# Kernel optimization log

Hardware: AMD Instinct MI355X
Metric: run time of the kernel (lower is better)

## Reference

```python
import jax, jax.numpy as jnp
import numpy as np

N_NODES = 100000


def _sage_conv(x, src, dst, W_l, W_r, b, num_nodes):
    # PyG SAGEConv with mean aggregation:
    # out_i = (mean_{j: (j->i) in E} x_j) @ W_l + x_i @ W_r + b
    msg_sum = jax.ops.segment_sum(x[src], dst, num_segments=num_nodes)  # [N, F]
    deg = jax.ops.segment_sum(jnp.ones_like(src, dtype=x.dtype), dst, num_segments=num_nodes)
    agg = msg_sum / jnp.maximum(deg, 1.0)[:, None]
    return agg @ W_l + x @ W_r + b


def setup_inputs() -> dict:
    key = jax.random.key(0)
    k = jax.random.split(key, 7)
    F_IN, H, C = 128, 128, 14
    E = 1600000
    x = jax.random.normal(k[0], (N_NODES, F_IN), dtype=jnp.float32)
    edge_index = jax.random.randint(k[1], (2, E), 0, N_NODES, dtype=jnp.int64)
    s = 1.0 / np.sqrt(F_IN)
    W1_l = jax.random.normal(k[2], (F_IN, H), dtype=jnp.float32) * s
    W1_r = jax.random.normal(k[3], (F_IN, H), dtype=jnp.float32) * s
    b1 = jnp.zeros((H,), dtype=jnp.float32)
    sh = 1.0 / np.sqrt(H)
    W2_l = jax.random.normal(k[4], (H, C), dtype=jnp.float32) * sh
    W2_r = jax.random.normal(k[5], (H, C), dtype=jnp.float32) * sh
    b2 = jnp.zeros((C,), dtype=jnp.float32)
    return {"x": x, "edge_index": edge_index, "edge_SF_num": 6,
            "W1_l": W1_l, "W1_r": W1_r, "b1": b1,
            "W2_l": W2_l, "W2_r": W2_r, "b2": b2}


def reference(x, edge_index, edge_SF_num, W1_l, W1_r, b1, W2_l, W2_r, b2):
    src, dst = edge_index[0], edge_index[1]
    h = _sage_conv(x, src, dst, W1_l, W1_r, b1, N_NODES)
    h = jax.nn.relu(h)
    # dropout is identity at inference (training=False)
    out = _sage_conv(h, src, dst, W2_l, W2_r, b2, N_NODES)
    x_SF = jax.nn.log_softmax(out[:, :edge_SF_num], axis=1)
    x_Ptx = jax.nn.log_softmax(out[:, edge_SF_num:], axis=1)
    return (x_SF, x_Ptx)
```

## Files before the change

### kernel.cpp

```cpp
#include <hip/hip_runtime.h>
#include <hip/hip_bf16.h>

#define NN 100000
#define F 128
#define C_OUT 14
#define ZP 16
#define WIN 64
#define NWIN ((NN + WIN - 1) / WIN)
#define WCAP 1408
#define EBATCH 4096
#define HS 136

typedef __attribute__((ext_vector_type(8))) short v8s;
typedef __attribute__((ext_vector_type(4))) float v4f;
typedef __attribute__((ext_vector_type(2))) float v2f;

static __device__ __forceinline__ unsigned short f2bf(float f) {
    unsigned int u = __float_as_uint(f);
    unsigned int r = (u + 0x7fffu + ((u >> 16) & 1u)) >> 16;
    return (unsigned short)r;
}
static __device__ __forceinline__ unsigned int pack2(float a, float b) {
    return (unsigned int)f2bf(a) | ((unsigned int)f2bf(b) << 16);
}
static __device__ __forceinline__ void unpack2(unsigned int u, float& lo, float& hi) {
    lo = __uint_as_float(u << 16);
    hi = __uint_as_float(u & 0xffff0000u);
}
static __device__ __forceinline__ void accf8(const uint2 u, float* a) {
    v2f f0 = __builtin_amdgcn_cvt_pk_f32_fp8((int)u.x, false);
    a[0] += f0[0]; a[1] += f0[1];
    v2f f1 = __builtin_amdgcn_cvt_pk_f32_fp8((int)u.x, true);
    a[2] += f1[0]; a[3] += f1[1];
    v2f f2 = __builtin_amdgcn_cvt_pk_f32_fp8((int)u.y, false);
    a[4] += f2[0]; a[5] += f2[1];
    v2f f3 = __builtin_amdgcn_cvt_pk_f32_fp8((int)u.y, true);
    a[6] += f3[0]; a[7] += f3[1];
}
static __device__ __forceinline__ unsigned int bf4_to_fp8x4(const unsigned short* sp) {
    float f0, f1, f2, f3;
    unpack2(*(const unsigned int*)(sp + 0), f0, f1);
    unpack2(*(const unsigned int*)(sp + 2), f2, f3);
    unsigned int w = __builtin_amdgcn_cvt_pk_fp8_f32(f0, f1, 0, false);
    return __builtin_amdgcn_cvt_pk_fp8_f32(f2, f3, w, true);
}

__global__ __launch_bounds__(256) void bin_kernel(
    const int* __restrict__ src, const int* __restrict__ dst,
    unsigned* __restrict__ bucket, int* __restrict__ wcur, int E)
{
    __shared__ int cnt_s[NWIN];
    __shared__ int gbase_s[NWIN];
    const int t = threadIdx.x;
    for (int w = t; w < NWIN; w += 256) cnt_s[w] = 0;
    __syncthreads();

    int      wreg[16];
    unsigned ereg[16];
    const int e0 = blockIdx.x * EBATCH;
    #pragma unroll
    for (int j = 0; j < 16; ++j) {
        const int e = e0 + j * 256 + t;
        int w = -1; unsigned ent = 0;
        if (e < E) {
            const int d = dst[e];
            const int s = src[e];
            w   = d >> 6;
            ent = ((unsigned)(d & (WIN - 1)) << 17) | (unsigned)s;
            atomicAdd(&cnt_s[w], 1);
        }
        wreg[j] = w; ereg[j] = ent;
    }
    __syncthreads();
    for (int w = t; w < NWIN; w += 256) {
        const int c = cnt_s[w];
        gbase_s[w] = c ? atomicAdd(&wcur[w], c) : 0;
    }
    __syncthreads();
    for (int w = t; w < NWIN; w += 256) cnt_s[w] = 0;
    __syncthreads();
    #pragma unroll
    for (int j = 0; j < 16; ++j) {
        const int w = wreg[j];
        if (w >= 0) {
            const int pos = gbase_s[w] + atomicAdd(&cnt_s[w], 1);
            if (pos < WCAP) bucket[(size_t)w * WCAP + pos] = ereg[j];
        }
    }
}

__global__ __launch_bounds__(256) void wprep_kernel(
    const float* __restrict__ W1l, const float* __restrict__ W1r,
    const float* __restrict__ W2l, const float* __restrict__ W2r,
    unsigned short* __restrict__ Wb, unsigned short* __restrict__ W2t)
{
    const int idx = blockIdx.x * 256 + threadIdx.x;
    if (idx < 2 * 128 * 128) {
        const int c   = idx >> 14;
        const int rem = idx & 16383;
        const int n   = rem >> 7;
        const int k   = rem & 127;
        const float* W = c ? W1r : W1l;
        Wb[idx] = f2bf(W[k * 128 + n]);
    } else if (idx < 2 * 128 * 128 + 32 * 128) {
        const int j = idx - 2 * 128 * 128;
        const int n = j >> 7;
        const int k = j & 127;
        float wv = 0.0f;
        if (n < 16) { if (n < C_OUT) wv = W2l[k * C_OUT + n]; }
        else        { if (n - 16 < C_OUT) wv = W2r[k * C_OUT + (n - 16)]; }
        W2t[j] = f2bf(wv);
    }
}

#define KS 72
__global__ __launch_bounds__(256, 2) void pre1_kernel(
    const float* __restrict__ x, const unsigned short* __restrict__ Wb,
    const float* __restrict__ b1, unsigned char* __restrict__ pqa,
    unsigned short* __restrict__ pqs)
{
    __shared__ unsigned short lds[128 * KS + 256 * KS];
    unsigned short* A_s = lds;
    unsigned short* W_s = lds + 128 * KS;

    const int t    = threadIdx.x;
    const int m0   = blockIdx.x * 128;
    const int lane = t & 63;
    const int wave = t >> 6;
    const int lr   = lane & 15;
    const int quad = lane >> 4;
    const int nw0  = wave * 64;

    v4f acc[8][4];
    #pragma unroll
    for (int mt = 0; mt < 8; ++mt)
        #pragma unroll
        for (int nt = 0; nt < 4; ++nt)
            acc[mt][nt] = (v4f){0.f, 0.f, 0.f, 0.f};

    #pragma unroll
    for (int ph = 0; ph < 2; ++ph) {
        const int kh = ph * 64;
        if (ph) __syncthreads();

        {
            const int mi = t & 127;
            const int ko = (t >> 7) * 32;
            const int m  = m0 + mi;
            unsigned short* dp = &A_s[mi * KS + ko];
            if (m < NN) {
                const float4* sp = (const float4*)(x + (size_t)m * F + kh + ko);
                #pragma unroll
                for (int j = 0; j < 8; j += 2) {
                    const float4 f0 = sp[j], f1 = sp[j + 1];
                    uint4 o;
                    o.x = pack2(f0.x, f0.y); o.y = pack2(f0.z, f0.w);
                    o.z = pack2(f1.x, f1.y); o.w = pack2(f1.z, f1.w);
                    *(uint4*)(dp + j * 4) = o;
                }
            } else {
                #pragma unroll
                for (int j = 0; j < 4; ++j)
                    *(uint4*)(dp + j * 8) = make_uint4(0u, 0u, 0u, 0u);
            }
        }
        {
            const unsigned short* sp = Wb + (size_t)t * 128 + kh;
            unsigned short* dp = &W_s[t * KS];
            #pragma unroll
            for (int j = 0; j < 8; ++j)
                *(uint4*)(dp + j * 8) = *(const uint4*)(sp + j * 8);
        }
        __syncthreads();

        #pragma unroll
        for (int ks = 0; ks < 2; ++ks) {
            const int k0 = ks * 32 + quad * 8;
            const v8s b0 = *(const v8s*)&W_s[(nw0 +  0 + lr) * KS + k0];
            const v8s b1v= *(const v8s*)&W_s[(nw0 + 16 + lr) * KS + k0];
            const v8s b2 = *(const v8s*)&W_s[(nw0 + 32 + lr) * KS + k0];
            const v8s b3 = *(const v8s*)&W_s[(nw0 + 48 + lr) * KS + k0];
            #pragma unroll
            for (int mt = 0; mt < 8; ++mt) {
                const v8s a = *(const v8s*)&A_s[(mt * 16 + lr) * KS + k0];
                acc[mt][0] = __builtin_amdgcn_mfma_f32_16x16x32_bf16(a, b0,  acc[mt][0], 0, 0, 0);
                acc[mt][1] = __builtin_amdgcn_mfma_f32_16x16x32_bf16(a, b1v, acc[mt][1], 0, 0, 0);
                acc[mt][2] = __builtin_amdgcn_mfma_f32_16x16x32_bf16(a, b2,  acc[mt][2], 0, 0, 0);
                acc[mt][3] = __builtin_amdgcn_mfma_f32_16x16x32_bf16(a, b3,  acc[mt][3], 0, 0, 0);
            }
        }
        __syncthreads();
    }

    float bias[4];
    #pragma unroll
    for (int nt = 0; nt < 4; ++nt) {
        const int n = nw0 + nt * 16 + lr;
        bias[nt] = (n >= 128) ? b1[n - 128] : 0.0f;
    }

    unsigned short* C_s = lds;
    #pragma unroll
    for (int p = 0; p < 2; ++p) {
        if ((nw0 >> 7) == p) {
            #pragma unroll
            for (int mt = 0; mt < 8; ++mt)
                #pragma unroll
                for (int nt = 0; nt < 4; ++nt) {
                    const int n = (nw0 & 127) + nt * 16 + lr;
                    #pragma unroll
                    for (int r = 0; r < 4; ++r) {
                        const int m = mt * 16 + quad * 4 + r;
                        C_s[m * 136 + n] = f2bf(acc[mt][nt][r] + bias[nt]);
                    }
                }
        }
        __syncthreads();
        if (p == 0) {
            const int mi8 = t >> 1;
            const int c0  = (t & 1) * 64;
            const int m   = m0 + mi8;
            if (m < NN) {
                unsigned char* dp = pqa + (size_t)m * 128 + c0;
                #pragma unroll
                for (int j = 0; j < 4; ++j) {
                    const unsigned short* sp = &C_s[mi8 * 136 + c0 + j * 16];
                    uint4 w;
                    w.x = bf4_to_fp8x4(sp + 0);
                    w.y = bf4_to_fp8x4(sp + 4);
                    w.z = bf4_to_fp8x4(sp + 8);
                    w.w = bf4_to_fp8x4(sp + 12);
                    *(uint4*)(dp + j * 16) = w;
                }
            }
        } else {
            const int mi = t & 127;
            const int nh = (t >> 7) * 64;
            const int m  = m0 + mi;
            if (m < NN) {
                unsigned short* dp = pqs + (size_t)m * 128 + nh;
                const unsigned short* sp = &C_s[mi * 136 + nh];
                #pragma unroll
                for (int j = 0; j < 8; ++j)
                    *(uint4*)(dp + j * 8) = *(const uint4*)(sp + j * 8);
            }
        }
        __syncthreads();
    }
}

__global__ __launch_bounds__(256, 5) void agg1f_kernel(
    const unsigned char* __restrict__ pqa, const unsigned short* __restrict__ pqs,
    unsigned* __restrict__ bucket, const int* __restrict__ wcur,
    const unsigned short* __restrict__ W2t, const float* __restrict__ b2,
    int* __restrict__ wbase, unsigned short* __restrict__ z, float* __restrict__ r)
{
    __shared__ unsigned list[WCAP];
    __shared__ int cnt_s[WIN], base_s[WIN], cur_s[WIN];
    __shared__ unsigned short hsm[WIN * HS];
    __shared__ unsigned short W2s[32 * HS];
    const int t  = threadIdx.x;
    const int wb = blockIdx.x;
    const int cntw = min(wcur[wb], WCAP);
    unsigned* bp = bucket + (size_t)wb * WCAP;

    {
        const int row = t >> 3;
        const int c16 = (t & 7) * 16;
        *(uint4*)&W2s[row * HS + c16]     = *(const uint4*)&W2t[row * 128 + c16];
        *(uint4*)&W2s[row * HS + c16 + 8] = *(const uint4*)&W2t[row * 128 + c16 + 8];
    }

    if (t < WIN) cnt_s[t] = 0;
    __syncthreads();
    for (int i = t; i < cntw; i += 256) atomicAdd(&cnt_s[bp[i] >> 17], 1);
    __syncthreads();
    if (t < WIN) base_s[t] = cnt_s[t];
    __syncthreads();
    for (int off = 1; off < WIN; off <<= 1) {
        int v = 0;
        if (t < WIN && t >= off) v = base_s[t - off];
        __syncthreads();
        if (t < WIN) base_s[t] += v;
        __syncthreads();
    }
    if (t < WIN) { const int b = base_s[t] - cnt_s[t]; base_s[t] = b; cur_s[t] = b; }
    __syncthreads();
    for (int i = t; i < cntw; i += 256) {
        const unsigned e = bp[i];
        list[atomicAdd(&cur_s[e >> 17], 1)] = e & 0x1FFFFu;
    }
    __syncthreads();

    for (int i = t; i < cntw; i += 256) bp[i] = list[i];
    if (t < WIN) wbase[wb * WIN + t] = base_s[t];

    const int g    = t >> 4;
    const int lane = t & 15;
    const int col  = lane * 8;
    #pragma unroll
    for (int rep = 0; rep < 4; ++rep) {
        const int nloc = rep * 16 + g;
        const int n = wb * WIN + nloc;
        if (n >= NN) continue;
        const int start = base_s[nloc];
        const int len   = cnt_s[nloc];
        float a0[8] = {0,0,0,0,0,0,0,0};
        float a1[8] = {0,0,0,0,0,0,0,0};
        float a2[8] = {0,0,0,0,0,0,0,0};
        float a3[8] = {0,0,0,0,0,0,0,0};
        int i = 0;
        for (; i + 8 <= len; i += 8) {
            const int s0 = (int)list[start + i + 0];
            const int s1 = (int)list[start + i + 1];
            const int s2 = (int)list[start + i + 2];
            const int s3 = (int)list[start + i + 3];
            const int s4 = (int)list[start + i + 4];
            const int s5 = (int)list[start + i + 5];
            const int s6 = (int)list[start + i + 6];
            const int s7 = (int)list[start + i + 7];
            const uint2 u0 = *(const uint2*)(pqa + (size_t)s0 * 128 + col);
            const uint2 u1 = *(const uint2*)(pqa + (size_t)s1 * 128 + col);
            const uint2 u2 = *(const uint2*)(pqa + (size_t)s2 * 128 + col);
            const uint2 u3 = *(const uint2*)(pqa + (size_t)s3 * 128 + col);
            const uint2 u4 = *(const uint2*)(pqa + (size_t)s4 * 128 + col);
            const uint2 u5 = *(const uint2*)(pqa + (size_t)s5 * 128 + col);
            const uint2 u6 = *(const uint2*)(pqa + (size_t)s6 * 128 + col);
            const uint2 u7 = *(const uint2*)(pqa + (size_t)s7 * 128 + col);
            accf8(u0, a0); accf8(u1, a1); accf8(u2, a2); accf8(u3, a3);
            accf8(u4, a0); accf8(u5, a1); accf8(u6, a2); accf8(u7, a3);
        }
        for (; i + 4 <= len; i += 4) {
            const int s0 = (int)list[start + i + 0];
            const int s1 = (int)list[start + i + 1];
            const int s2 = (int)list[start + i + 2];
            const int s3 = (int)list[start + i + 3];
            const uint2 u0 = *(const uint2*)(pqa + (size_t)s0 * 128 + col);
            const uint2 u1 = *(const uint2*)(pqa + (size_t)s1 * 128 + col);
            const uint2 u2 = *(const uint2*)(pqa + (size_t)s2 * 128 + col);
            const uint2 u3 = *(const uint2*)(pqa + (size_t)s3 * 128 + col);
            accf8(u0, a0); accf8(u1, a1); accf8(u2, a2); accf8(u3, a3);
        }
        for (; i < len; ++i) {
            const int s = (int)list[start + i];
            const uint2 u = *(const uint2*)(pqa + (size_t)s * 128 + col);
            accf8(u, a0);
        }
        const float inv = 1.0f / (float)max(len, 1);
        const uint4 uq = *(const uint4*)(pqs + (size_t)n * 128 + col);
        float q[8];
        unpack2(uq.x, q[0], q[1]); unpack2(uq.y, q[2], q[3]);
        unpack2(uq.z, q[4], q[5]); unpack2(uq.w, q[6], q[7]);
        float hv[8];
        #pragma unroll
        for (int j = 0; j < 8; ++j)
            hv[j] = fmaxf((a0[j] + a1[j] + a2[j] + a3[j]) * inv + q[j], 0.0f);
        uint4 o;
        o.x = pack2(hv[0], hv[1]);
        o.y = pack2(hv[2], hv[3]);
        o.z = pack2(hv[4], hv[5]);
        o.w = pack2(hv[6], hv[7]);
        *(uint4*)&hsm[nloc * HS + col] = o;
    }
    __syncthreads();

    {
        const int wave = t >> 6;
        const int l64  = t & 63;
        const int lr   = l64 & 15;
        const int quad = l64 >> 4;
        const int m0w  = wave * 16;
        v4f accz = (v4f){0.f, 0.f, 0.f, 0.f};
        v4f accr = (v4f){0.f, 0.f, 0.f, 0.f};
        #pragma unroll
        for (int kt = 0; kt < 4; ++kt) {
            const int k0 = kt * 32 + quad * 8;
            const v8s a  = *(const v8s*)&hsm[(m0w + lr) * HS + k0];
            const v8s bz = *(const v8s*)&W2s[lr * HS + k0];
            const v8s br = *(const v8s*)&W2s[(16 + lr) * HS + k0];
            accz = __builtin_amdgcn_mfma_f32_16x16x32_bf16(a, bz, accz, 0, 0, 0);
            accr = __builtin_amdgcn_mfma_f32_16x16x32_bf16(a, br, accr, 0, 0, 0);
        }
        const float b2v = (lr < C_OUT) ? b2[lr] : 0.0f;
        #pragma unroll
        for (int rr = 0; rr < 4; ++rr) {
            const int m = m0w + quad * 4 + rr;
            const int n = wb * WIN + m;
            if (n < NN) {
                z[(size_t)n * ZP + lr] = f2bf(accz[rr]);
                r[(size_t)n * ZP + lr] = accr[rr] + b2v;
            }
        }
    }
}

__global__ __launch_bounds__(256) void agg2s_kernel(
    const unsigned short* __restrict__ z, const float* __restrict__ r,
    const unsigned* __restrict__ bucket, const int* __restrict__ wcur,
    const int* __restrict__ wbase, const int* __restrict__ sf_ptr,
    float* __restrict__ out)
{
    __shared__ unsigned list[WCAP];
    __shared__ int base_s[WIN + 1];
    __shared__ float sm[WIN][ZP + 1];
    const int t  = threadIdx.x;
    const int wb = blockIdx.x;
    const int cntw = min(wcur[wb], WCAP);
    const unsigned* bp = bucket + (size_t)wb * WCAP;

    if (t < WIN) base_s[t] = wbase[wb * WIN + t];
    if (t == 0) base_s[WIN] = cntw;
    for (int i = t; i < cntw; i += 256) list[i] = bp[i];
    __syncthreads();

    const int g  = t >> 2;
    const int j4 = (t & 3) * 4;
    const int n  = wb * WIN + g;
    if (n < NN) {
        const int start = base_s[g];
        const int len   = base_s[g + 1] - base_s[g];
        float4 a0 = make_float4(0.f, 0.f, 0.f, 0.f);
        float4 a1 = a0, a2 = a0, a3 = a0;
        int i = 0;
        for (; i + 4 <= len; i += 4) {
            const int s0 = (int)list[start + i + 0];
            const int s1 = (int)list[start + i + 1];
            const int s2 = (int)list[start + i + 2];
            const int s3 = (int)list[start + i + 3];
            const uint2 u0 = *(const uint2*)(z + (size_t)s0 * ZP + j4);
            const uint2 u1 = *(const uint2*)(z + (size_t)s1 * ZP + j4);
            const uint2 u2 = *(const uint2*)(z + (size_t)s2 * ZP + j4);
            const uint2 u3 = *(const uint2*)(z + (size_t)s3 * ZP + j4);
            float f0, f1, f2, f3;
            unpack2(u0.x, f0, f1); unpack2(u0.y, f2, f3);
            a0.x += f0; a0.y += f1; a0.z += f2; a0.w += f3;
            unpack2(u1.x, f0, f1); unpack2(u1.y, f2, f3);
            a1.x += f0; a1.y += f1; a1.z += f2; a1.w += f3;
            unpack2(u2.x, f0, f1); unpack2(u2.y, f2, f3);
            a2.x += f0; a2.y += f1; a2.z += f2; a2.w += f3;
            unpack2(u3.x, f0, f1); unpack2(u3.y, f2, f3);
            a3.x += f0; a3.y += f1; a3.z += f2; a3.w += f3;
        }
        for (; i < len; ++i) {
            const int s = (int)list[start + i];
            const uint2 u = *(const uint2*)(z + (size_t)s * ZP + j4);
            float f0, f1, f2, f3;
            unpack2(u.x, f0, f1); unpack2(u.y, f2, f3);
            a0.x += f0; a0.y += f1; a0.z += f2; a0.w += f3;
        }
        const float inv = 1.0f / (float)max(len, 1);
        const float4 rv = *(const float4*)(r + (size_t)n * ZP + j4);
        sm[g][j4 + 0] = (a0.x + a1.x + a2.x + a3.x) * inv + rv.x;
        sm[g][j4 + 1] = (a0.y + a1.y + a2.y + a3.y) * inv + rv.y;
        sm[g][j4 + 2] = (a0.z + a1.z + a2.z + a3.z) * inv + rv.z;
        sm[g][j4 + 3] = (a0.w + a1.w + a2.w + a3.w) * inv + rv.w;
    }
    __syncthreads();

    if (t < WIN) {
        const int n2 = wb * WIN + t;
        if (n2 < NN) {
            const int sf = *sf_ptr;
            const float* row = sm[t];
            float m = -1e30f;
            for (int c = 0; c < sf; ++c) m = fmaxf(m, row[c]);
            float s = 0.0f;
            for (int c = 0; c < sf; ++c) s += expf(row[c] - m);
            float ls = m + logf(s);
            for (int c = 0; c < sf; ++c)
                out[(long long)n2 * sf + c] = row[c] - ls;
            m = -1e30f;
            for (int c = sf; c < C_OUT; ++c) m = fmaxf(m, row[c]);
            s = 0.0f;
            for (int c = sf; c < C_OUT; ++c) s += expf(row[c] - m);
            ls = m + logf(s);
            const int pt = C_OUT - sf;
            for (int c = sf; c < C_OUT; ++c)
                out[(long long)NN * sf + (long long)n2 * pt + (c - sf)] = row[c] - ls;
        }
    }
}

extern "C" void kernel_launch(void* const* d_in, const int* in_sizes, int n_in,
                              void* d_out, int out_size, void* d_ws, size_t ws_size,
                              hipStream_t stream)
{
    const float* x   = (const float*)d_in[0];
    const int*   ei  = (const int*)d_in[1];
    const int*   sfp = (const int*)d_in[2];
    const float* W1l = (const float*)d_in[3];
    const float* W1r = (const float*)d_in[4];
    const float* b1  = (const float*)d_in[5];
    const float* W2l = (const float*)d_in[6];
    const float* W2r = (const float*)d_in[7];
    const float* b2  = (const float*)d_in[8];
    float*       out = (float*)d_out;

    const int E = in_sizes[1] / 2;
    const int* src = ei;
    const int* dst = ei + E;

    int*      wcur   = (int*)d_ws;
    int*      wbase  = wcur + 2048;
    unsigned* bucket = (unsigned*)(wbase + NWIN * WIN);
    unsigned short* Wb  = (unsigned short*)(bucket + (size_t)NWIN * WCAP);
    unsigned short* W2t = Wb + 2 * 128 * 128;
    unsigned short* pqs = W2t + 32 * 128;
    unsigned char*  pqa = (unsigned char*)(pqs + (size_t)NN * 128);
    unsigned short* z   = (unsigned short*)(pqa + (size_t)NN * 128);
    float*          r   = (float*)(z + (size_t)NN * ZP);

    hipMemsetAsync(wcur, 0, 2048 * sizeof(int), stream);

    bin_kernel<<<(E + EBATCH - 1) / EBATCH, 256, 0, stream>>>(src, dst, bucket, wcur, E);

    wprep_kernel<<<(2 * 128 * 128 + 32 * 128 + 255) / 256, 256, 0, stream>>>(
        W1l, W1r, W2l, W2r, Wb, W2t);

    pre1_kernel<<<(NN + 127) / 128, 256, 0, stream>>>(x, Wb, b1, pqa, pqs);

    agg1f_kernel<<<NWIN, 256, 0, stream>>>(pqa, pqs, bucket, wcur, W2t, b2, wbase, z, r);

    agg2s_kernel<<<NWIN, 256, 0, stream>>>(z, r, bucket, wcur, wbase, sfp, out);
}
```

Measured before the change: 223.6 us.

## Hold W1 fragments in registers and shrink pre1 tile to 64 rows

The first-layer projection kernel now loads its weight fragments straight from global memory into registers instead of staging them in LDS. It processes 64 rows per block over the full K in one pass, which cuts LDS use and removes the two-phase K loop and its barriers, and it raises the occupancy hint to 3. This trades more register pressure and more blocks, each re-reading the weights, for less LDS traffic and synchronisation. Separately, the layer-2 gather loop in the aggregation kernel is unrolled to 8 edges per iteration so more loads are in flight.

```diff
diff --git a/kernel.cpp b/kernel.cpp
--- a/kernel.cpp
+++ b/kernel.cpp
@@ -113,84 +113,72 @@
     }
 }
 
-#define KS 72
-__global__ __launch_bounds__(256, 2) void pre1_kernel(
+#define KSA 136
+__global__ __launch_bounds__(256, 3) void pre1_kernel(
     const float* __restrict__ x, const unsigned short* __restrict__ Wb,
     const float* __restrict__ b1, unsigned char* __restrict__ pqa,
     unsigned short* __restrict__ pqs)
 {
-    __shared__ unsigned short lds[128 * KS + 256 * KS];
-    unsigned short* A_s = lds;
-    unsigned short* W_s = lds + 128 * KS;
+    __shared__ unsigned short A_s[64 * KSA];
 
     const int t    = threadIdx.x;
-    const int m0   = blockIdx.x * 128;
+    const int m0   = blockIdx.x * 64;
     const int lane = t & 63;
     const int wave = t >> 6;
     const int lr   = lane & 15;
     const int quad = lane >> 4;
     const int nw0  = wave * 64;
 
-    v4f acc[8][4];
-    #pragma unroll
-    for (int mt = 0; mt < 8; ++mt)
+    v8s bf[4][4];
+    #pragma unroll
+    for (int nt = 0; nt < 4; ++nt)
+        #pragma unroll
+        for (int ks = 0; ks < 4; ++ks)
+            bf[nt][ks] = *(const v8s*)(Wb + (size_t)(nw0 + nt * 16 + lr) * 128 + ks * 32 + quad * 8);
+
+    {
+        const int mi = t & 63;
+        const int ko = (t >> 6) * 32;
+        const int m  = m0 + mi;
+        unsigned short* dp = &A_s[mi * KSA + ko];
+        if (m < NN) {
+            const float4* sp = (const float4*)(x + (size_t)m * F + ko);
+            #pragma unroll
+            for (int j = 0; j < 8; j += 2) {
+                const float4 f0 = sp[j], f1 = sp[j + 1];
+                uint4 o;
+                o.x = pack2(f0.x, f0.y); o.y = pack2(f0.z, f0.w);
+                o.z = pack2(f1.x, f1.y); o.w = pack2(f1.z, f1.w);
+                *(uint4*)(dp + j * 4) = o;
+            }
+        } else {
+            #pragma unroll
+            for (int j = 0; j < 4; ++j)
+                *(uint4*)(dp + j * 8) = make_uint4(0u, 0u, 0u, 0u);
+        }
+    }
+    __syncthreads();
+
+    v4f acc[4][4];
+    #pragma unroll
+    for (int mt = 0; mt < 4; ++mt)
         #pragma unroll
         for (int nt = 0; nt < 4; ++nt)
             acc[mt][nt] = (v4f){0.f, 0.f, 0.f, 0.f};
 
     #pragma unroll
-    for (int ph = 0; ph < 2; ++ph) {
-        const int kh = ph * 64;
-        if (ph) __syncthreads();
-
-        {
-            const int mi = t & 127;
-            const int ko = (t >> 7) * 32;
-            const int m  = m0 + mi;
-            unsigned short* dp = &A_s[mi * KS + ko];
-            if (m < NN) {
-                const float4* sp = (const float4*)(x + (size_t)m * F + kh + ko);
-                #pragma unroll
-                for (int j = 0; j < 8; j += 2) {
-                    const float4 f0 = sp[j], f1 = sp[j + 1];
-                    uint4 o;
-                    o.x = pack2(f0.x, f0.y); o.y = pack2(f0.z, f0.w);
-                    o.z = pack2(f1.x, f1.y); o.w = pack2(f1.z, f1.w);
-                    *(uint4*)(dp + j * 4) = o;
-                }
-            } else {
-                #pragma unroll
-                for (int j = 0; j < 4; ++j)
-                    *(uint4*)(dp + j * 8) = make_uint4(0u, 0u, 0u, 0u);
-            }
-        }
-        {
-            const unsigned short* sp = Wb + (size_t)t * 128 + kh;
-            unsigned short* dp = &W_s[t * KS];
-            #pragma unroll
-            for (int j = 0; j < 8; ++j)
-                *(uint4*)(dp + j * 8) = *(const uint4*)(sp + j * 8);
-        }
-        __syncthreads();
-
+    for (int ks = 0; ks < 4; ++ks) {
+        const int k0 = ks * 32 + quad * 8;
         #pragma unroll
-        for (int ks = 0; ks < 2; ++ks) {
-            const int k0 = ks * 32 + quad * 8;
-            const v8s b0 = *(const v8s*)&W_s[(nw0 +  0 + lr) * KS + k0];
-            const v8s b1v= *(const v8s*)&W_s[(nw0 + 16 + lr) * KS + k0];
-            const v8s b2 = *(const v8s*)&W_s[(nw0 + 32 + lr) * KS + k0];
-            const v8s b3 = *(const v8s*)&W_s[(nw0 + 48 + lr) * KS + k0];
-            #pragma unroll
-            for (int mt = 0; mt < 8; ++mt) {
-                const v8s a = *(const v8s*)&A_s[(mt * 16 + lr) * KS + k0];
-                acc[mt][0] = __builtin_amdgcn_mfma_f32_16x16x32_bf16(a, b0,  acc[mt][0], 0, 0, 0);
-                acc[mt][1] = __builtin_amdgcn_mfma_f32_16x16x32_bf16(a, b1v, acc[mt][1], 0, 0, 0);
-                acc[mt][2] = __builtin_amdgcn_mfma_f32_16x16x32_bf16(a, b2,  acc[mt][2], 0, 0, 0);
-                acc[mt][3] = __builtin_amdgcn_mfma_f32_16x16x32_bf16(a, b3,  acc[mt][3], 0, 0, 0);
-            }
-        }
-        __syncthreads();
-    }
+        for (int mt = 0; mt < 4; ++mt) {
+            const v8s a = *(const v8s*)&A_s[(mt * 16 + lr) * KSA + k0];
+            acc[mt][0] = __builtin_amdgcn_mfma_f32_16x16x32_bf16(a, bf[0][ks], acc[mt][0], 0, 0, 0);
+            acc[mt][1] = __builtin_amdgcn_mfma_f32_16x16x32_bf16(a, bf[1][ks], acc[mt][1], 0, 0, 0);
+            acc[mt][2] = __builtin_amdgcn_mfma_f32_16x16x32_bf16(a, bf[2][ks], acc[mt][2], 0, 0, 0);
+            acc[mt][3] = __builtin_amdgcn_mfma_f32_16x16x32_bf16(a, bf[3][ks], acc[mt][3], 0, 0, 0);
+        }
+    }
+    __syncthreads();
 
     float bias[4];
     #pragma unroll
@@ -199,32 +187,32 @@
         bias[nt] = (n >= 128) ? b1[n - 128] : 0.0f;
     }
 
-    unsigned short* C_s = lds;
+    unsigned short* C_s = A_s;
     #pragma unroll
     for (int p = 0; p < 2; ++p) {
         if ((nw0 >> 7) == p) {
             #pragma unroll
-            for (int mt = 0; mt < 8; ++mt)
+            for (int mt = 0; mt < 4; ++mt)
                 #pragma unroll
                 for (int nt = 0; nt < 4; ++nt) {
                     const int n = (nw0 & 127) + nt * 16 + lr;
                     #pragma unroll
                     for (int r = 0; r < 4; ++r) {
                         const int m = mt * 16 + quad * 4 + r;
-                        C_s[m * 136 + n] = f2bf(acc[mt][nt][r] + bias[nt]);
+                        C_s[m * KSA + n] = f2bf(acc[mt][nt][r] + bias[nt]);
                     }
                 }
         }
         __syncthreads();
         if (p == 0) {
-            const int mi8 = t >> 1;
-            const int c0  = (t & 1) * 64;
+            const int mi8 = t >> 2;
+            const int c0  = (t & 3) * 32;
             const int m   = m0 + mi8;
             if (m < NN) {
                 unsigned char* dp = pqa + (size_t)m * 128 + c0;
                 #pragma unroll
-                for (int j = 0; j < 4; ++j) {
-                    const unsigned short* sp = &C_s[mi8 * 136 + c0 + j * 16];
+                for (int j = 0; j < 2; ++j) {
+                    const unsigned short* sp = &C_s[mi8 * KSA + c0 + j * 16];
                     uint4 w;
                     w.x = bf4_to_fp8x4(sp + 0);
                     w.y = bf4_to_fp8x4(sp + 4);
@@ -234,14 +222,14 @@
                 }
             }
         } else {
-            const int mi = t & 127;
-            const int nh = (t >> 7) * 64;
+            const int mi = t >> 2;
+            const int c0 = (t & 3) * 32;
             const int m  = m0 + mi;
             if (m < NN) {
-                unsigned short* dp = pqs + (size_t)m * 128 + nh;
-                const unsigned short* sp = &C_s[mi * 136 + nh];
+                unsigned short* dp = pqs + (size_t)m * 128 + c0;
+                const unsigned short* sp = &C_s[mi * KSA + c0];
                 #pragma unroll
-                for (int j = 0; j < 8; ++j)
+                for (int j = 0; j < 4; ++j)
                     *(uint4*)(dp + j * 8) = *(const uint4*)(sp + j * 8);
             }
         }
@@ -422,6 +410,41 @@
         float4 a0 = make_float4(0.f, 0.f, 0.f, 0.f);
         float4 a1 = a0, a2 = a0, a3 = a0;
         int i = 0;
+        for (; i + 8 <= len; i += 8) {
+            const int s0 = (int)list[start + i + 0];
+            const int s1 = (int)list[start + i + 1];
+            const int s2 = (int)list[start + i + 2];
+            const int s3 = (int)list[start + i + 3];
+            const int s4 = (int)list[start + i + 4];
+            const int s5 = (int)list[start + i + 5];
+            const int s6 = (int)list[start + i + 6];
+            const int s7 = (int)list[start + i + 7];
+            const uint2 u0 = *(const uint2*)(z + (size_t)s0 * ZP + j4);
+            const uint2 u1 = *(const uint2*)(z + (size_t)s1 * ZP + j4);
+            const uint2 u2 = *(const uint2*)(z + (size_t)s2 * ZP + j4);
+            const uint2 u3 = *(const uint2*)(z + (size_t)s3 * ZP + j4);
+            const uint2 u4 = *(const uint2*)(z + (size_t)s4 * ZP + j4);
+            const uint2 u5 = *(const uint2*)(z + (size_t)s5 * ZP + j4);
+            const uint2 u6 = *(const uint2*)(z + (size_t)s6 * ZP + j4);
+            const uint2 u7 = *(const uint2*)(z + (size_t)s7 * ZP + j4);
+            float f0, f1, f2, f3;
+            unpack2(u0.x, f0, f1); unpack2(u0.y, f2, f3);
+            a0.x += f0; a0.y += f1; a0.z += f2; a0.w += f3;
+            unpack2(u1.x, f0, f1); unpack2(u1.y, f2, f3);
+            a1.x += f0; a1.y += f1; a1.z += f2; a1.w += f3;
+            unpack2(u2.x, f0, f1); unpack2(u2.y, f2, f3);
+            a2.x += f0; a2.y += f1; a2.z += f2; a2.w += f3;
+            unpack2(u3.x, f0, f1); unpack2(u3.y, f2, f3);
+            a3.x += f0; a3.y += f1; a3.z += f2; a3.w += f3;
+            unpack2(u4.x, f0, f1); unpack2(u4.y, f2, f3);
+            a0.x += f0; a0.y += f1; a0.z += f2; a0.w += f3;
+            unpack2(u5.x, f0, f1); unpack2(u5.y, f2, f3);
+            a1.x += f0; a1.y += f1; a1.z += f2; a1.w += f3;
+            unpack2(u6.x, f0, f1); unpack2(u6.y, f2, f3);
+            a2.x += f0; a2.y += f1; a2.z += f2; a2.w += f3;
+            unpack2(u7.x, f0, f1); unpack2(u7.y, f2, f3);
+            a3.x += f0; a3.y += f1; a3.z += f2; a3.w += f3;
+        }
         for (; i + 4 <= len; i += 4) {
             const int s0 = (int)list[start + i + 0];
             const int s1 = (int)list[start + i + 1];
@@ -517,7 +540,7 @@
     wprep_kernel<<<(2 * 128 * 128 + 32 * 128 + 255) / 256, 256, 0, stream>>>(
         W1l, W1r, W2l, W2r, Wb, W2t);
 
-    pre1_kernel<<<(NN + 127) / 128, 256, 0, stream>>>(x, Wb, b1, pqa, pqs);
+    pre1_kernel<<<(NN + 63) / 64, 256, 0, stream>>>(x, Wb, b1, pqa, pqs);
 
     agg1f_kernel<<<NWIN, 256, 0, stream>>>(pqa, pqs, bucket, wcur, W2t, b2, wbase, z, r);
 
```

Measured after the change: 219.0 us. 1.02x faster.
